# Optimization experiments

Hardware: AMD Instinct MI355X
Metric: run time of the kernel (lower is better)

Reference implementation:

```python
import jax, jax.numpy as jnp
import numpy as np

H, E, DFF = 1024, 8, 4096


def setup_inputs() -> dict:
    key = jax.random.key(0)
    ks = jax.random.split(key, 7)
    s = lambda *shape: 1.0 / np.sqrt(shape[-2] if len(shape) > 1 else shape[-1])
    x = jax.random.normal(ks[0], (2, 2048, H), dtype=jnp.float32)
    Wr = jax.random.normal(ks[1], (H, E), dtype=jnp.float32) * (1.0 / np.sqrt(H))
    br = jnp.zeros((E,), dtype=jnp.float32)
    W1 = jax.random.normal(ks[2], (E, H, DFF), dtype=jnp.float32) * (1.0 / np.sqrt(H))
    b1 = jnp.zeros((E, DFF), dtype=jnp.float32)
    W2 = jax.random.normal(ks[3], (E, DFF, H), dtype=jnp.float32) * (1.0 / np.sqrt(DFF))
    b2 = jnp.zeros((E, H), dtype=jnp.float32)
    return {"x": x, "Wr": Wr, "br": br, "W1": W1, "b1": b1, "W2": W2, "b2": b2}


def reference(x, Wr, br, W1, b1, W2, b2):
    B, S, Hd = x.shape
    n_exp = W1.shape[0]
    xt = x.reshape(-1, Hd)                      # (T, H)
    logits = xt @ Wr + br                       # (T, E)
    probs = jax.nn.softmax(logits, axis=-1)
    gate = jnp.max(probs, axis=-1)              # (T,) top-1 gate value
    idx = jnp.argmax(probs, axis=-1)            # (T,) chosen expert
    # dense all-expert FFN, then one-hot combine (vectorized equivalent of per-token loop)
    h1 = jnp.maximum(jnp.einsum('th,ehf->etf', xt, W1) + b1[:, None, :], 0.0)  # (E,T,DFF)
    ye = jnp.einsum('etf,efh->eth', h1, W2) + b2[:, None, :]                   # (E,T,H)
    onehot = jax.nn.one_hot(idx, n_exp, dtype=xt.dtype)                        # (T,E)
    y = jnp.einsum('te,eth->th', onehot, ye) * gate[:, None]                   # (T,H)
    return y.reshape(B, S, Hd)
```

## Files before the change

### kernel.cpp

```cpp
#include <hip/hip_runtime.h>
#include <stdint.h>

typedef unsigned short u16;
typedef __attribute__((ext_vector_type(8))) short s16x8;
typedef __attribute__((ext_vector_type(4))) float f32x4;
typedef __attribute__((ext_vector_type(4))) unsigned uint4v;

#define NEXP 8
#define HD 1024
#define DFF 4096
#define BM 128
#define BN 128
#define BK 64

#define TILE_U16 (BM * BK)

__device__ __forceinline__ u16 f2bf(float f) {
  union { float f; unsigned u; } c; c.f = f;
  unsigned r = c.u + 0x7fffu + ((c.u >> 16) & 1u);
  return (u16)(r >> 16);
}

__device__ __forceinline__ unsigned cvtpk(float a, float b) {
  unsigned r;
  asm("v_cvt_pk_bf16_f32 %0, %1, %2" : "=v"(r) : "v"(a), "v"(b));
  return r;
}

__device__ __forceinline__ void gload_lds16(const void* g, const void* l) {
  __builtin_amdgcn_global_load_lds(
      (const __attribute__((address_space(1))) unsigned int*)(uintptr_t)g,
      (__attribute__((address_space(3))) unsigned int*)(unsigned)(uintptr_t)l,
      16, 0, 0);
}

template <int K, int N>
__device__ __forceinline__ void convt_gl(const float* __restrict__ W,
    u16* __restrict__ Wt, int idx, float* __restrict__ Tf) {
  const int e = idx >> 9;
  const int ti = idx & 511;
  const int k0 = (ti % (K / 128)) * 128;
  const int n0 = (ti / (K / 128)) * 64;
  const int t = threadIdx.x;
  const float* src = W + (size_t)e * K * N + (size_t)k0 * N + n0;
#pragma unroll
  for (int c = 0; c < 8; ++c) {
    int slot = c * 256 + t;
    gload_lds16(src + (size_t)(slot >> 4) * N + (slot & 15) * 4, Tf + slot * 4);
  }
  __syncthreads();
  const int n = t >> 2, ks = t & 3;
  float v[32];
#pragma unroll
  for (int j = 0; j < 32; ++j)
    v[j] = Tf[(ks * 32 + j) * 64 + n];
  uint4v q0, q1, q2, q3;
#pragma unroll
  for (int a = 0; a < 4; ++a) {
    q0[a] = cvtpk(v[2 * a], v[2 * a + 1]);
    q1[a] = cvtpk(v[8 + 2 * a], v[9 + 2 * a]);
    q2[a] = cvtpk(v[16 + 2 * a], v[17 + 2 * a]);
    q3[a] = cvtpk(v[24 + 2 * a], v[25 + 2 * a]);
  }
  u16* d = Wt + (size_t)e * K * N + (size_t)(n0 + n) * K + k0 + ks * 32;
  *(uint4v*)d = q0;
  *(uint4v*)(d + 8) = q1;
  *(uint4v*)(d + 16) = q2;
  *(uint4v*)(d + 24) = q3;
}

__global__ __launch_bounds__(256) void prep1_k(
    const float* __restrict__ x, const float* __restrict__ Wr,
    const float* __restrict__ br,
    int* __restrict__ tok_exp, float* __restrict__ tok_gate,
    const float* __restrict__ W1, u16* __restrict__ W1t,
    u16* __restrict__ Xbf, int T) {
  __shared__ __align__(16) float Tf[128 * 64];
  const int bid = blockIdx.x;
  const int NBR = T / 4;
  if (bid >= NBR) {
    convt_gl<HD, DFF>(W1, W1t, bid - NBR, Tf);
    return;
  }
  const int w = threadIdx.x >> 6, l = threadIdx.x & 63;
  const int t = bid * 4 + w;
  const float4* xr = (const float4*)(x + (size_t)t * HD);
  float acc[NEXP];
#pragma unroll
  for (int j = 0; j < NEXP; ++j) acc[j] = 0.f;
#pragma unroll
  for (int i = 0; i < 4; ++i) {
    float4 v = xr[l + i * 64];
    unsigned pa = cvtpk(v.x, v.y), pb = cvtpk(v.z, v.w);
    *(uint2*)&Xbf[(size_t)t * HD + (l + i * 64) * 4] = make_uint2(pa, pb);
    const int h = (l + i * 64) * 4;
    const float* w0 = Wr + (size_t)h * NEXP;
#pragma unroll
    for (int c = 0; c < 4; ++c) {
      float xv = (c == 0) ? v.x : (c == 1) ? v.y : (c == 2) ? v.z : v.w;
      const float4* wr4 = (const float4*)(w0 + c * NEXP);
      float4 a = wr4[0], b = wr4[1];
      acc[0] += xv * a.x; acc[1] += xv * a.y; acc[2] += xv * a.z; acc[3] += xv * a.w;
      acc[4] += xv * b.x; acc[5] += xv * b.y; acc[6] += xv * b.z; acc[7] += xv * b.w;
    }
  }
#pragma unroll
  for (int j = 0; j < NEXP; ++j)
#pragma unroll
    for (int off = 32; off > 0; off >>= 1) acc[j] += __shfl_xor(acc[j], off);
  if (l == 0) {
    float lg[NEXP];
    float best = acc[0] + br[0]; int bi = 0;
    lg[0] = best;
#pragma unroll
    for (int j = 1; j < NEXP; ++j) {
      lg[j] = acc[j] + br[j];
      if (lg[j] > best) { best = lg[j]; bi = j; }
    }
    float s = 0.f;
#pragma unroll
    for (int j = 0; j < NEXP; ++j) s += expf(lg[j] - best);
    tok_exp[t] = bi;
    tok_gate[t] = 1.0f / s;
  }
}

__global__ __launch_bounds__(64) void scan_k(const int* __restrict__ tok_exp, int T,
    int* __restrict__ seg, int* __restrict__ cursor,
    int* __restrict__ ntile, int* __restrict__ tile_e, int* __restrict__ tile_m) {
  const int l = threadIdx.x;
  int cnt[NEXP];
#pragma unroll
  for (int j = 0; j < NEXP; ++j) cnt[j] = 0;
  for (int i = l; i < T; i += 64) {
    int e = tok_exp[i];
#pragma unroll
    for (int j = 0; j < NEXP; ++j) cnt[j] += (e == j) ? 1 : 0;
  }
#pragma unroll
  for (int j = 0; j < NEXP; ++j)
#pragma unroll
    for (int off = 32; off > 0; off >>= 1) cnt[j] += __shfl_xor(cnt[j], off);
  if (l == 0) {
    int s = 0, nt = 0;
#pragma unroll
    for (int e = 0; e < NEXP; ++e) {
      seg[e] = s; cursor[e] = s;
      int c = cnt[e];
      for (int m = 0; m < c; m += BM) { tile_e[nt] = e; tile_m[nt] = m; ++nt; }
      s += c;
    }
    seg[NEXP] = s;
    ntile[0] = nt;
  }
}

__global__ __launch_bounds__(256) void gather_k(const u16* __restrict__ Xbf,
    const int* __restrict__ tok_exp, const float* __restrict__ tok_gate,
    int* __restrict__ cursor, int* __restrict__ perm, float* __restrict__ gatep,
    u16* __restrict__ Xg) {
  const int w = threadIdx.x >> 6, l = threadIdx.x & 63;
  const int t = blockIdx.x * 4 + w;
  int pos = 0;
  if (l == 0) {
    int e = tok_exp[t];
    pos = atomicAdd(&cursor[e], 1);
    perm[pos] = t;
    gatep[pos] = tok_gate[t];
  }
  pos = __shfl(pos, 0);
  const s16x8* srcr = (const s16x8*)(Xbf + (size_t)t * HD);
  s16x8* dst = (s16x8*)(Xg + (size_t)pos * HD);
#pragma unroll
  for (int i = 0; i < HD / 8 / 64; ++i)
    dst[l + i * 64] = srcr[l + i * 64];
}

template <int KD, int ND, int EPI, int KSPLIT>
__device__ __forceinline__ void gemm_body(
    u16* __restrict__ sh,
    const u16* __restrict__ A, const u16* __restrict__ Bt,
    const float* __restrict__ bias, const int* __restrict__ seg,
    const int* __restrict__ ntile, const int* __restrict__ tile_e,
    const int* __restrict__ tile_m,
    u16* __restrict__ H1out, float* __restrict__ Pt,
    int bx, int by, int ks) {
  if (by >= ntile[0]) return;
  const int e  = tile_e[by];
  const int m0 = tile_m[by];
  const int s0 = seg[e];
  const int cnt = seg[e + 1] - s0;
  const int n0 = bx * BN;
  constexpr int NT = (KD / KSPLIT) / BK;
  const int kbase = ks * (KD / KSPLIT);

  const int t = threadIdx.x;
  const int l = t & 63, w = t >> 6;
  const int wr = w >> 1, wc = w & 1;

  const f32x4 fzero = {0.f, 0.f, 0.f, 0.f};
  f32x4 acc[4][4];
#pragma unroll
  for (int i = 0; i < 4; ++i)
#pragma unroll
    for (int j = 0; j < 4; ++j) acc[i][j] = fzero;

  const int sub = t & 7, r8 = t >> 3;
  const int koff = (sub ^ (r8 & 7)) * 8;
  int aoff[4], boff[4];
  const u16* bte = Bt + (size_t)e * ND * KD;
#pragma unroll
  for (int c = 0; c < 4; ++c) {
    int row = c * 32 + r8;
    int rg = m0 + row; if (rg >= cnt) rg = cnt - 1;
    aoff[c] = (s0 + rg) * KD + kbase + koff;
    boff[c] = (n0 + row) * KD + kbase + koff;
  }

  u16* Ac = sh;
  u16* Bc = sh + TILE_U16;
  u16* An = sh + 2 * TILE_U16;
  u16* Bn = sh + 3 * TILE_U16;

#define STAGE(pa, pb, tt) do { \
    const int ko_ = (tt) * BK; \
    _Pragma("unroll") for (int c_ = 0; c_ < 4; ++c_) \
      gload_lds16(A + (size_t)aoff[c_] + ko_, (pa) + (c_ * 256 + t) * 8); \
    _Pragma("unroll") for (int c_ = 0; c_ < 4; ++c_) \
      gload_lds16(bte + (size_t)boff[c_] + ko_, (pb) + (c_ * 256 + t) * 8); \
  } while (0)

#define COMPUTE(pa, pb) do { \
    _Pragma("unroll") for (int s_ = 0; s_ < 2; ++s_) { \
      const int fo_ = ((s_ * 4 + (l >> 4)) ^ (l & 7)) * 8; \
      s16x8 af_[4], bf_[4]; \
      _Pragma("unroll") for (int mi_ = 0; mi_ < 4; ++mi_) \
        af_[mi_] = *(const s16x8*)&(pa)[(wr * 64 + mi_ * 16 + (l & 15)) * BK + fo_]; \
      _Pragma("unroll") for (int ni_ = 0; ni_ < 4; ++ni_) \
        bf_[ni_] = *(const s16x8*)&(pb)[(wc * 64 + ni_ * 16 + (l & 15)) * BK + fo_]; \
      _Pragma("unroll") for (int mi_ = 0; mi_ < 4; ++mi_) \
        _Pragma("unroll") for (int ni_ = 0; ni_ < 4; ++ni_) \
          acc[mi_][ni_] = __builtin_amdgcn_mfma_f32_16x16x32_bf16(af_[mi_], bf_[ni_], acc[mi_][ni_], 0, 0, 0); \
    } \
  } while (0)

  STAGE(Ac, Bc, 0);
  __syncthreads();
  for (int tt = 0; tt < NT; ++tt) {
    if (tt + 1 < NT) STAGE(An, Bn, tt + 1);
    COMPUTE(Ac, Bc);
    if (tt + 1 < NT) {
      __syncthreads();
      u16* xp;
      xp = Ac; Ac = An; An = xp;
      xp = Bc; Bc = Bn; Bn = xp;
    }
  }

#undef STAGE
#undef COMPUTE

  const int lr = (l >> 4) * 4;
  const int lc = l & 15;

  if constexpr (EPI == 0) {
    float bv2[4];
#pragma unroll
    for (int ni = 0; ni < 4; ++ni)
      bv2[ni] = bias[(size_t)e * ND + n0 + wc * 64 + ni * 16 + lc];
#pragma unroll
    for (int mi = 0; mi < 4; ++mi) {
#pragma unroll
      for (int r = 0; r < 4; ++r) {
        int row = m0 + wr * 64 + mi * 16 + lr + r;
        if (row < cnt) {
          u16* hrow = H1out + (size_t)(s0 + row) * ND + n0 + wc * 64;
#pragma unroll
          for (int ni = 0; ni < 4; ++ni) {
            float v = acc[mi][ni][r] + bv2[ni];
            v = v > 0.f ? v : 0.f;
            hrow[ni * 16 + lc] = f2bf(v);
          }
        }
      }
    }
  } else {
    const int totT = seg[NEXP];
#pragma unroll
    for (int mi = 0; mi < 4; ++mi) {
#pragma unroll
      for (int r = 0; r < 4; ++r) {
        int row = m0 + wr * 64 + mi * 16 + lr + r;
        if (row < cnt) {
          float* prow = Pt + ((size_t)ks * totT + s0 + row) * ND + n0 + wc * 64;
#pragma unroll
          for (int ni = 0; ni < 4; ++ni)
            prow[ni * 16 + lc] = acc[mi][ni][r];
        }
      }
    }
  }
}

__global__ __launch_bounds__(256, 2) void gemm1_fused_k(
    const u16* __restrict__ Xg, const u16* __restrict__ W1t,
    const float* __restrict__ b1, const int* __restrict__ seg,
    const int* __restrict__ ntile, const int* __restrict__ tile_e,
    const int* __restrict__ tile_m, u16* __restrict__ H1,
    const float* __restrict__ W2, u16* __restrict__ W2t, int ng1) {
  __shared__ __align__(16) u16 sh[4 * TILE_U16];
  const int bid = blockIdx.x;
  if (bid < ng1) {
    gemm_body<HD, DFF, 0, 1>(sh, Xg, W1t, b1, seg, ntile, tile_e,
                             tile_m, H1, nullptr, bid % (DFF / BN), bid / (DFF / BN), 0);
  } else {
    convt_gl<DFF, HD>(W2, W2t, bid - ng1, (float*)sh);
  }
}

__global__ __launch_bounds__(256, 2) void gemm2_k(
    const u16* __restrict__ H1, const u16* __restrict__ W2t,
    const int* __restrict__ seg, const int* __restrict__ ntile,
    const int* __restrict__ tile_e, const int* __restrict__ tile_m,
    float* __restrict__ Pt) {
  __shared__ __align__(16) u16 sh[4 * TILE_U16];
  gemm_body<DFF, HD, 2, 4>(sh, H1, W2t, nullptr, seg, ntile, tile_e,
                           tile_m, nullptr, Pt, blockIdx.x, blockIdx.y, blockIdx.z);
}

__global__ __launch_bounds__(256) void reduce_k(const float* __restrict__ Pt,
    const float* __restrict__ b2, const int* __restrict__ perm,
    const float* __restrict__ gatep, const int* __restrict__ tok_exp,
    float* __restrict__ out) {
  const int pos = blockIdx.x;
  const int totT = gridDim.x;
  const int tok = perm[pos];
  const float g = gatep[pos];
  const int e = tok_exp[tok];
  const int h = threadIdx.x * 4;
  float4 s = *(const float4*)(Pt + ((size_t)0 * totT + pos) * HD + h);
#pragma unroll
  for (int k = 1; k < 4; ++k) {
    float4 p = *(const float4*)(Pt + ((size_t)k * totT + pos) * HD + h);
    s.x += p.x; s.y += p.y; s.z += p.z; s.w += p.w;
  }
  float4 b = *(const float4*)(b2 + (size_t)e * HD + h);
  float4 o;
  o.x = (s.x + b.x) * g; o.y = (s.y + b.y) * g;
  o.z = (s.z + b.z) * g; o.w = (s.w + b.w) * g;
  *(float4*)(out + (size_t)tok * HD + h) = o;
}

extern "C" void kernel_launch(void* const* d_in, const int* in_sizes, int n_in,
                              void* d_out, int out_size, void* d_ws, size_t ws_size,
                              hipStream_t stream) {
  const float* x  = (const float*)d_in[0];
  const float* Wr = (const float*)d_in[1];
  const float* br = (const float*)d_in[2];
  const float* W1 = (const float*)d_in[3];
  const float* b1 = (const float*)d_in[4];
  const float* W2 = (const float*)d_in[5];
  const float* b2 = (const float*)d_in[6];
  float* out = (float*)d_out;

  const int T = in_sizes[0] / HD;
  char* ws = (char*)d_ws;
  int*   cursor   = (int*)(ws + 64);
  int*   seg      = (int*)(ws + 128);
  int*   ntile    = (int*)(ws + 192);
  int*   tile_e   = (int*)(ws + 256);
  int*   tile_m   = (int*)(ws + 512);
  int*   tok_exp  = (int*)(ws + 1024);
  float* tok_gate = (float*)(ws + 1024 + 4 * (size_t)T);
  int*   perm     = (int*)(ws + 1024 + 8 * (size_t)T);
  float* gatep    = (float*)(ws + 1024 + 12 * (size_t)T);
  u16*   Xg       = (u16*)(ws + 1024 + 16 * (size_t)T);
  u16*   H1       = (u16*)(ws + 1024 + 16 * (size_t)T + 2 * (size_t)T * HD);
  size_t off2     = 1024 + 16 * (size_t)T + 2 * (size_t)T * HD + 2 * (size_t)T * DFF;
  u16*   W1t      = (u16*)(ws + off2);
  u16*   W2t      = (u16*)(ws + off2 + 2 * (size_t)NEXP * HD * DFF);
  float* Pt       = (float*)W1t;
  u16*   Xbf      = H1;

  const int NBR = T / 4;
  const int NCT = 512 * NEXP;
  hipLaunchKernelGGL(prep1_k, dim3(NBR + NCT), dim3(256), 0, stream,
                     x, Wr, br, tok_exp, tok_gate, W1, W1t, Xbf, T);
  hipLaunchKernelGGL(scan_k, dim3(1), dim3(64), 0, stream,
                     tok_exp, T, seg, cursor, ntile, tile_e, tile_m);
  hipLaunchKernelGGL(gather_k, dim3(T / 4), dim3(256), 0, stream,
                     Xbf, tok_exp, tok_gate, cursor, perm, gatep, Xg);
  const int maxtile = (T + BM - 1) / BM + NEXP - 1;
  const int ng1 = (DFF / BN) * maxtile;
  hipLaunchKernelGGL(gemm1_fused_k, dim3(ng1 + NCT), dim3(256), 0, stream,
                     Xg, W1t, b1, seg, ntile, tile_e, tile_m, H1, W2, W2t, ng1);
  hipLaunchKernelGGL(gemm2_k, dim3(HD / BN, maxtile, 4), dim3(256), 0, stream,
                     H1, W2t, seg, ntile, tile_e, tile_m, Pt);
  hipLaunchKernelGGL(reduce_k, dim3(T), dim3(256), 0, stream, Pt, b2, perm, gatep, tok_exp, out);
}
```

Measured before the change: 290.2 us.

## Fuse split-K reduction and gating into GEMM2 epilogue via atomic adds

Removes the separate reduce kernel and the fp32 partial-sum buffer. GEMM2 now scatters gated, bias-added results directly into the output with atomicAdd, after a memset of the output. This saves writing and re-reading four partial planes and one launch, at the cost of atomic traffic and nondeterministic summation order. It also changes the thread mapping in the W2 transpose-convert so that consecutive lanes read consecutive LDS columns.

```diff
diff --git a/kernel.cpp b/kernel.cpp
--- a/kernel.cpp
+++ b/kernel.cpp
@@ -49,7 +49,7 @@
     gload_lds16(src + (size_t)(slot >> 4) * N + (slot & 15) * 4, Tf + slot * 4);
   }
   __syncthreads();
-  const int n = t >> 2, ks = t & 3;
+  const int n = t & 63, ks = t >> 6;
   float v[32];
 #pragma unroll
   for (int j = 0; j < 32; ++j)
@@ -183,7 +183,8 @@
     const float* __restrict__ bias, const int* __restrict__ seg,
     const int* __restrict__ ntile, const int* __restrict__ tile_e,
     const int* __restrict__ tile_m,
-    u16* __restrict__ H1out, float* __restrict__ Pt,
+    u16* __restrict__ H1out, float* __restrict__ Yout,
+    const int* __restrict__ perm, const float* __restrict__ gatep,
     int bx, int by, int ks) {
   if (by >= ntile[0]) return;
   const int e  = tile_e[by];
@@ -262,12 +263,12 @@
 
   const int lr = (l >> 4) * 4;
   const int lc = l & 15;
+  float bv2[4];
+#pragma unroll
+  for (int ni = 0; ni < 4; ++ni)
+    bv2[ni] = bias[(size_t)e * ND + n0 + wc * 64 + ni * 16 + lc];
 
   if constexpr (EPI == 0) {
-    float bv2[4];
-#pragma unroll
-    for (int ni = 0; ni < 4; ++ni)
-      bv2[ni] = bias[(size_t)e * ND + n0 + wc * 64 + ni * 16 + lc];
 #pragma unroll
     for (int mi = 0; mi < 4; ++mi) {
 #pragma unroll
@@ -285,17 +286,21 @@
       }
     }
   } else {
-    const int totT = seg[NEXP];
 #pragma unroll
     for (int mi = 0; mi < 4; ++mi) {
 #pragma unroll
       for (int r = 0; r < 4; ++r) {
         int row = m0 + wr * 64 + mi * 16 + lr + r;
         if (row < cnt) {
-          float* prow = Pt + ((size_t)ks * totT + s0 + row) * ND + n0 + wc * 64;
-#pragma unroll
-          for (int ni = 0; ni < 4; ++ni)
-            prow[ni * 16 + lc] = acc[mi][ni][r];
+          int tok = perm[s0 + row];
+          float g = gatep[s0 + row];
+          float* orow = Yout + (size_t)tok * ND + n0 + wc * 64;
+#pragma unroll
+          for (int ni = 0; ni < 4; ++ni) {
+            float v = acc[mi][ni][r];
+            if (ks == 0) v += bv2[ni];
+            atomicAdd(&orow[ni * 16 + lc], v * g);
+          }
         }
       }
     }
@@ -311,8 +316,9 @@
   __shared__ __align__(16) u16 sh[4 * TILE_U16];
   const int bid = blockIdx.x;
   if (bid < ng1) {
-    gemm_body<HD, DFF, 0, 1>(sh, Xg, W1t, b1, seg, ntile, tile_e,
-                             tile_m, H1, nullptr, bid % (DFF / BN), bid / (DFF / BN), 0);
+    gemm_body<HD, DFF, 0, 1>(sh, Xg, W1t, b1, seg, ntile, tile_e, tile_m,
+                             H1, nullptr, nullptr, nullptr,
+                             bid % (DFF / BN), bid / (DFF / BN), 0);
   } else {
     convt_gl<DFF, HD>(W2, W2t, bid - ng1, (float*)sh);
   }
@@ -320,35 +326,14 @@
 
 __global__ __launch_bounds__(256, 2) void gemm2_k(
     const u16* __restrict__ H1, const u16* __restrict__ W2t,
-    const int* __restrict__ seg, const int* __restrict__ ntile,
-    const int* __restrict__ tile_e, const int* __restrict__ tile_m,
-    float* __restrict__ Pt) {
+    const float* __restrict__ b2, const int* __restrict__ seg,
+    const int* __restrict__ ntile, const int* __restrict__ tile_e,
+    const int* __restrict__ tile_m, float* __restrict__ out,
+    const int* __restrict__ perm, const float* __restrict__ gatep) {
   __shared__ __align__(16) u16 sh[4 * TILE_U16];
-  gemm_body<DFF, HD, 2, 4>(sh, H1, W2t, nullptr, seg, ntile, tile_e,
-                           tile_m, nullptr, Pt, blockIdx.x, blockIdx.y, blockIdx.z);
-}
-
-__global__ __launch_bounds__(256) void reduce_k(const float* __restrict__ Pt,
-    const float* __restrict__ b2, const int* __restrict__ perm,
-    const float* __restrict__ gatep, const int* __restrict__ tok_exp,
-    float* __restrict__ out) {
-  const int pos = blockIdx.x;
-  const int totT = gridDim.x;
-  const int tok = perm[pos];
-  const float g = gatep[pos];
-  const int e = tok_exp[tok];
-  const int h = threadIdx.x * 4;
-  float4 s = *(const float4*)(Pt + ((size_t)0 * totT + pos) * HD + h);
-#pragma unroll
-  for (int k = 1; k < 4; ++k) {
-    float4 p = *(const float4*)(Pt + ((size_t)k * totT + pos) * HD + h);
-    s.x += p.x; s.y += p.y; s.z += p.z; s.w += p.w;
-  }
-  float4 b = *(const float4*)(b2 + (size_t)e * HD + h);
-  float4 o;
-  o.x = (s.x + b.x) * g; o.y = (s.y + b.y) * g;
-  o.z = (s.z + b.z) * g; o.w = (s.w + b.w) * g;
-  *(float4*)(out + (size_t)tok * HD + h) = o;
+  gemm_body<DFF, HD, 1, 4>(sh, H1, W2t, b2, seg, ntile, tile_e, tile_m,
+                           nullptr, out, perm, gatep,
+                           blockIdx.x, blockIdx.y, blockIdx.z);
 }
 
 extern "C" void kernel_launch(void* const* d_in, const int* in_sizes, int n_in,
@@ -379,9 +364,9 @@
   size_t off2     = 1024 + 16 * (size_t)T + 2 * (size_t)T * HD + 2 * (size_t)T * DFF;
   u16*   W1t      = (u16*)(ws + off2);
   u16*   W2t      = (u16*)(ws + off2 + 2 * (size_t)NEXP * HD * DFF);
-  float* Pt       = (float*)W1t;
   u16*   Xbf      = H1;
 
+  hipMemsetAsync(out, 0, (size_t)out_size * sizeof(float), stream);
   const int NBR = T / 4;
   const int NCT = 512 * NEXP;
   hipLaunchKernelGGL(prep1_k, dim3(NBR + NCT), dim3(256), 0, stream,
@@ -395,6 +380,5 @@
   hipLaunchKernelGGL(gemm1_fused_k, dim3(ng1 + NCT), dim3(256), 0, stream,
                      Xg, W1t, b1, seg, ntile, tile_e, tile_m, H1, W2, W2t, ng1);
   hipLaunchKernelGGL(gemm2_k, dim3(HD / BN, maxtile, 4), dim3(256), 0, stream,
-                     H1, W2t, seg, ntile, tile_e, tile_m, Pt);
-  hipLaunchKernelGGL(reduce_k, dim3(T), dim3(256), 0, stream, Pt, b2, perm, gatep, tok_exp, out);
-}
+                     H1, W2t, b2, seg, ntile, tile_e, tile_m, out, perm, gatep);
+}
```

Result: slower. 321.9 us (+11.0%).

## Replace token gather copy with indexed A-loads in GEMM1, halve GEMM2 split-K

Applied to the files above, without the earlier changes.

Drops the kernel that copied bf16 token rows into expert-sorted order. GEMM1 now reads activation rows straight from the unsorted bf16 buffer through the perm index, and a lightweight kernel only builds perm and the gate values. GEMM2 split-K goes from 4 to 2, which halves the partial-sum traffic in the reduce but gives fewer blocks. The W2 transpose thread mapping is also changed so consecutive threads read consecutive LDS columns.

```diff
diff --git a/kernel.cpp b/kernel.cpp
--- a/kernel.cpp
+++ b/kernel.cpp
@@ -49,7 +49,7 @@
     gload_lds16(src + (size_t)(slot >> 4) * N + (slot & 15) * 4, Tf + slot * 4);
   }
   __syncthreads();
-  const int n = t >> 2, ks = t & 3;
+  const int n = t & 63, ks = t >> 6;
   float v[32];
 #pragma unroll
   for (int j = 0; j < 32; ++j)
@@ -155,34 +155,23 @@
   }
 }
 
-__global__ __launch_bounds__(256) void gather_k(const u16* __restrict__ Xbf,
-    const int* __restrict__ tok_exp, const float* __restrict__ tok_gate,
-    int* __restrict__ cursor, int* __restrict__ perm, float* __restrict__ gatep,
-    u16* __restrict__ Xg) {
-  const int w = threadIdx.x >> 6, l = threadIdx.x & 63;
-  const int t = blockIdx.x * 4 + w;
-  int pos = 0;
-  if (l == 0) {
-    int e = tok_exp[t];
-    pos = atomicAdd(&cursor[e], 1);
-    perm[pos] = t;
-    gatep[pos] = tok_gate[t];
-  }
-  pos = __shfl(pos, 0);
-  const s16x8* srcr = (const s16x8*)(Xbf + (size_t)t * HD);
-  s16x8* dst = (s16x8*)(Xg + (size_t)pos * HD);
-#pragma unroll
-  for (int i = 0; i < HD / 8 / 64; ++i)
-    dst[l + i * 64] = srcr[l + i * 64];
-}
-
-template <int KD, int ND, int EPI, int KSPLIT>
+__global__ __launch_bounds__(256) void gatherlite_k(const int* __restrict__ tok_exp,
+    const float* __restrict__ tok_gate, int* __restrict__ cursor,
+    int* __restrict__ perm, float* __restrict__ gatep) {
+  const int t = blockIdx.x * 256 + threadIdx.x;
+  int e = tok_exp[t];
+  int pos = atomicAdd(&cursor[e], 1);
+  perm[pos] = t;
+  gatep[pos] = tok_gate[t];
+}
+
+template <int KD, int ND, int EPI, int KSPLIT, bool AIND>
 __device__ __forceinline__ void gemm_body(
     u16* __restrict__ sh,
     const u16* __restrict__ A, const u16* __restrict__ Bt,
     const float* __restrict__ bias, const int* __restrict__ seg,
     const int* __restrict__ ntile, const int* __restrict__ tile_e,
-    const int* __restrict__ tile_m,
+    const int* __restrict__ tile_m, const int* __restrict__ perm,
     u16* __restrict__ H1out, float* __restrict__ Pt,
     int bx, int by, int ks) {
   if (by >= ntile[0]) return;
@@ -213,7 +202,10 @@
   for (int c = 0; c < 4; ++c) {
     int row = c * 32 + r8;
     int rg = m0 + row; if (rg >= cnt) rg = cnt - 1;
-    aoff[c] = (s0 + rg) * KD + kbase + koff;
+    int arow;
+    if constexpr (AIND) arow = perm[s0 + rg];
+    else arow = s0 + rg;
+    aoff[c] = arow * KD + kbase + koff;
     boff[c] = (n0 + row) * KD + kbase + koff;
   }
 
@@ -303,16 +295,18 @@
 }
 
 __global__ __launch_bounds__(256, 2) void gemm1_fused_k(
-    const u16* __restrict__ Xg, const u16* __restrict__ W1t,
+    const u16* __restrict__ Xbf, const u16* __restrict__ W1t,
     const float* __restrict__ b1, const int* __restrict__ seg,
     const int* __restrict__ ntile, const int* __restrict__ tile_e,
-    const int* __restrict__ tile_m, u16* __restrict__ H1,
+    const int* __restrict__ tile_m, const int* __restrict__ perm,
+    u16* __restrict__ H1,
     const float* __restrict__ W2, u16* __restrict__ W2t, int ng1) {
   __shared__ __align__(16) u16 sh[4 * TILE_U16];
   const int bid = blockIdx.x;
   if (bid < ng1) {
-    gemm_body<HD, DFF, 0, 1>(sh, Xg, W1t, b1, seg, ntile, tile_e,
-                             tile_m, H1, nullptr, bid % (DFF / BN), bid / (DFF / BN), 0);
+    gemm_body<HD, DFF, 0, 1, true>(sh, Xbf, W1t, b1, seg, ntile, tile_e, tile_m,
+                                   perm, H1, nullptr,
+                                   bid % (DFF / BN), bid / (DFF / BN), 0);
   } else {
     convt_gl<DFF, HD>(W2, W2t, bid - ng1, (float*)sh);
   }
@@ -324,8 +318,9 @@
     const int* __restrict__ tile_e, const int* __restrict__ tile_m,
     float* __restrict__ Pt) {
   __shared__ __align__(16) u16 sh[4 * TILE_U16];
-  gemm_body<DFF, HD, 2, 4>(sh, H1, W2t, nullptr, seg, ntile, tile_e,
-                           tile_m, nullptr, Pt, blockIdx.x, blockIdx.y, blockIdx.z);
+  gemm_body<DFF, HD, 2, 2, false>(sh, H1, W2t, nullptr, seg, ntile, tile_e,
+                                  tile_m, nullptr, nullptr, Pt,
+                                  blockIdx.x, blockIdx.y, blockIdx.z);
 }
 
 __global__ __launch_bounds__(256) void reduce_k(const float* __restrict__ Pt,
@@ -339,11 +334,8 @@
   const int e = tok_exp[tok];
   const int h = threadIdx.x * 4;
   float4 s = *(const float4*)(Pt + ((size_t)0 * totT + pos) * HD + h);
-#pragma unroll
-  for (int k = 1; k < 4; ++k) {
-    float4 p = *(const float4*)(Pt + ((size_t)k * totT + pos) * HD + h);
-    s.x += p.x; s.y += p.y; s.z += p.z; s.w += p.w;
-  }
+  float4 p = *(const float4*)(Pt + ((size_t)1 * totT + pos) * HD + h);
+  s.x += p.x; s.y += p.y; s.z += p.z; s.w += p.w;
   float4 b = *(const float4*)(b2 + (size_t)e * HD + h);
   float4 o;
   o.x = (s.x + b.x) * g; o.y = (s.y + b.y) * g;
@@ -374,13 +366,12 @@
   float* tok_gate = (float*)(ws + 1024 + 4 * (size_t)T);
   int*   perm     = (int*)(ws + 1024 + 8 * (size_t)T);
   float* gatep    = (float*)(ws + 1024 + 12 * (size_t)T);
-  u16*   Xg       = (u16*)(ws + 1024 + 16 * (size_t)T);
+  u16*   Xbf      = (u16*)(ws + 1024 + 16 * (size_t)T);
   u16*   H1       = (u16*)(ws + 1024 + 16 * (size_t)T + 2 * (size_t)T * HD);
   size_t off2     = 1024 + 16 * (size_t)T + 2 * (size_t)T * HD + 2 * (size_t)T * DFF;
   u16*   W1t      = (u16*)(ws + off2);
   u16*   W2t      = (u16*)(ws + off2 + 2 * (size_t)NEXP * HD * DFF);
   float* Pt       = (float*)W1t;
-  u16*   Xbf      = H1;
 
   const int NBR = T / 4;
   const int NCT = 512 * NEXP;
@@ -388,13 +379,13 @@
                      x, Wr, br, tok_exp, tok_gate, W1, W1t, Xbf, T);
   hipLaunchKernelGGL(scan_k, dim3(1), dim3(64), 0, stream,
                      tok_exp, T, seg, cursor, ntile, tile_e, tile_m);
-  hipLaunchKernelGGL(gather_k, dim3(T / 4), dim3(256), 0, stream,
-                     Xbf, tok_exp, tok_gate, cursor, perm, gatep, Xg);
+  hipLaunchKernelGGL(gatherlite_k, dim3(T / 256), dim3(256), 0, stream,
+                     tok_exp, tok_gate, cursor, perm, gatep);
   const int maxtile = (T + BM - 1) / BM + NEXP - 1;
   const int ng1 = (DFF / BN) * maxtile;
   hipLaunchKernelGGL(gemm1_fused_k, dim3(ng1 + NCT), dim3(256), 0, stream,
-                     Xg, W1t, b1, seg, ntile, tile_e, tile_m, H1, W2, W2t, ng1);
-  hipLaunchKernelGGL(gemm2_k, dim3(HD / BN, maxtile, 4), dim3(256), 0, stream,
+                     Xbf, W1t, b1, seg, ntile, tile_e, tile_m, perm, H1, W2, W2t, ng1);
+  hipLaunchKernelGGL(gemm2_k, dim3(HD / BN, maxtile, 2), dim3(256), 0, stream,
                      H1, W2t, seg, ntile, tile_e, tile_m, Pt);
   hipLaunchKernelGGL(reduce_k, dim3(T), dim3(256), 0, stream, Pt, b2, perm, gatep, tok_exp, out);
 }
```

Result: faster. 255.8 us (-11.8%).
